# Kernel optimization log

Measured on AMD Instinct MI355X. Metric: run time of the kernel, lower is better.

## Reference

```python
import jax, jax.numpy as jnp
import numpy as np

B, T, C, H = 2, 2048, 1024, 16
HD = C // H
EPS = 1e-5


def _gelu_tanh(x):
    # 0.5*x*(1+tanh(sqrt(2/pi)*(x+0.044715*x^3)))
    c = jnp.sqrt(jnp.asarray(2.0 / np.pi, dtype=x.dtype))
    return 0.5 * x * (1.0 + jnp.tanh(c * (x + 0.044715 * x * x * x)))


def _layernorm(x, g, b):
    mu = jnp.mean(x, axis=-1, keepdims=True)
    var = jnp.mean(jnp.square(x - mu), axis=-1, keepdims=True)
    return (x - mu) * jax.lax.rsqrt(var + EPS) * g + b


def setup_inputs() -> dict:
    key = jax.random.key(0)
    ks = jax.random.split(key, 8)
    s = lambda fan_in: 1.0 / np.sqrt(fan_in)
    return {
        "x": jax.random.normal(ks[0], (B, T, C), jnp.float32),
        "ln1_g": jnp.ones((C,), jnp.float32),
        "ln1_b": jnp.zeros((C,), jnp.float32),
        "W_attn": jax.random.normal(ks[1], (C, 3 * C), jnp.float32) * s(C),
        "b_attn": jnp.zeros((3 * C,), jnp.float32),
        "W_proj": jax.random.normal(ks[2], (C, C), jnp.float32) * s(C),
        "b_proj": jnp.zeros((C,), jnp.float32),
        "ln2_g": jnp.ones((C,), jnp.float32),
        "ln2_b": jnp.zeros((C,), jnp.float32),
        "W_fc": jax.random.normal(ks[3], (C, 4 * C), jnp.float32) * s(C),
        "b_fc": jnp.zeros((4 * C,), jnp.float32),
        "W_fc2": jax.random.normal(ks[4], (4 * C, C), jnp.float32) * s(4 * C),
        "b_fc2": jnp.zeros((C,), jnp.float32),
    }


def reference(x, ln1_g, ln1_b, W_attn, b_attn, W_proj, b_proj,
              ln2_g, ln2_b, W_fc, b_fc, W_fc2, b_fc2):
    # --- attention branch (pre-LN) ---
    h = _layernorm(x, ln1_g, ln1_b)
    qkv = h @ W_attn + b_attn                      # [B,T,3C]
    q, k, v = jnp.split(qkv, 3, axis=2)
    q = q.reshape(B, T, H, HD).transpose(0, 2, 1, 3)  # [B,H,T,HD]
    k = k.reshape(B, T, H, HD).transpose(0, 2, 1, 3)
    v = v.reshape(B, T, H, HD).transpose(0, 2, 1, 3)
    att = jnp.einsum('bhqd,bhkd->bhqk', q, k) / jnp.sqrt(jnp.asarray(HD, x.dtype))
    causal = jnp.tril(jnp.ones((T, T), bool))
    att = jnp.where(causal, att, jnp.asarray(-jnp.inf, att.dtype))
    att = jax.nn.softmax(att, axis=-1)
    y = jnp.einsum('bhqk,bhkd->bhqd', att, v)      # [B,H,T,HD]
    y = y.transpose(0, 2, 1, 3).reshape(B, T, C)
    x = x + (y @ W_proj + b_proj)
    # --- MLP branch (pre-LN) ---
    h = _layernorm(x, ln2_g, ln2_b)
    h = _gelu_tanh(h @ W_fc + b_fc)
    x = x + (h @ W_fc2 + b_fc2)
    return x
```

## Files before the change

### kernel.cpp

```cpp
#include <hip/hip_runtime.h>
#include <hip/hip_bf16.h>
#include <cstdint>
#include <cstddef>

#define B_  2
#define T_  2048
#define C_  1024
#define H_  16
#define HD_ 64
#define M_TOT 4096

typedef __bf16 bf16x8 __attribute__((ext_vector_type(8)));
typedef float  f32x4  __attribute__((ext_vector_type(4)));
typedef unsigned short u16;

__device__ __forceinline__ u16 f2bf(float f) {
  __hip_bfloat16 h = __float2bfloat16(f);
  return __builtin_bit_cast(u16, h);
}

__device__ __forceinline__ void async_cp16(const u16* g, u16* l) {
  __builtin_amdgcn_global_load_lds(
      (const __attribute__((address_space(1))) void*)g,
      (__attribute__((address_space(3))) void*)l, 16, 0, 0);
}

__device__ __forceinline__ float gelu_f(float x) {
  const float z = 0.7978845608028654f * (x + 0.044715f * x * x * x);
  return x / (1.0f + __expf(-2.0f * z));
}

__device__ __forceinline__ void ln_row(
    const float* __restrict__ x, const float* __restrict__ g,
    const float* __restrict__ b, u16* __restrict__ out, int row, int tid) {
  const float4 v = reinterpret_cast<const float4*>(x)[row * 256 + tid];
  float s  = v.x + v.y + v.z + v.w;
  float sq = v.x * v.x + v.y * v.y + v.z * v.z + v.w * v.w;
#pragma unroll
  for (int off = 32; off > 0; off >>= 1) {
    s  += __shfl_xor(s, off);
    sq += __shfl_xor(sq, off);
  }
  __shared__ float red[8];
  const int wave = tid >> 6;
  if ((tid & 63) == 0) { red[wave] = s; red[4 + wave] = sq; }
  __syncthreads();
  s  = red[0] + red[1] + red[2] + red[3];
  sq = red[4] + red[5] + red[6] + red[7];
  const float mu   = s * (1.0f / 1024.0f);
  const float rstd = rsqrtf(sq * (1.0f / 1024.0f) - mu * mu + 1e-5f);
  const float4 gv = reinterpret_cast<const float4*>(g)[tid];
  const float4 bv = reinterpret_cast<const float4*>(b)[tid];
  ushort4 o;
  o.x = f2bf((v.x - mu) * rstd * gv.x + bv.x);
  o.y = f2bf((v.y - mu) * rstd * gv.y + bv.y);
  o.z = f2bf((v.z - mu) * rstd * gv.z + bv.z);
  o.w = f2bf((v.w - mu) * rstd * gv.w + bv.w);
  reinterpret_cast<ushort4*>(out)[row * 256 + tid] = o;
}

__global__ __launch_bounds__(256) void ln_bf16_kernel(
    const float* __restrict__ x, const float* __restrict__ g,
    const float* __restrict__ b, u16* __restrict__ out) {
  ln_row(x, g, b, out, blockIdx.x, threadIdx.x);
}

__global__ __launch_bounds__(256) void prep_kernel(
    const float* __restrict__ x, const float* __restrict__ ln1_g,
    const float* __restrict__ ln1_b, u16* __restrict__ h1,
    const float* __restrict__ W_attn, u16* __restrict__ wt_attn,
    const float* __restrict__ W_proj, u16* __restrict__ wt_proj,
    const float* __restrict__ W_fc,   u16* __restrict__ wt_fc,
    const float* __restrict__ W_fc2,  u16* __restrict__ wt_fc2) {
  int bid = blockIdx.x;
  if (bid < 4096) { ln_row(x, ln1_g, ln1_b, h1, bid, threadIdx.x); return; }
  bid -= 4096;
  const float* W; u16* Wt; int K, N, nx;
  if (bid < 3072)      {              W = W_attn; Wt = wt_attn; K = 1024; N = 3072; nx = 96; }
  else if (bid < 4096) { bid -= 3072; W = W_proj; Wt = wt_proj; K = 1024; N = 1024; nx = 32; }
  else if (bid < 8192) { bid -= 4096; W = W_fc;   Wt = wt_fc;   K = 1024; N = 4096; nx = 128; }
  else                 { bid -= 8192; W = W_fc2;  Wt = wt_fc2;  K = 4096; N = 1024; nx = 32; }
  const int n0 = (bid % nx) * 32, k0 = (bid / nx) * 32;
  __shared__ float tile[32][33];
  const int tx = threadIdx.x & 31;
  const int ty = threadIdx.x >> 5;
#pragma unroll
  for (int i = 0; i < 4; ++i)
    tile[ty + 8 * i][tx] = W[(k0 + ty + 8 * i) * (size_t)N + n0 + tx];
  __syncthreads();
#pragma unroll
  for (int i = 0; i < 4; ++i)
    Wt[(n0 + ty + 8 * i) * (size_t)K + k0 + tx] = f2bf(tile[tx][ty + 8 * i]);
}

template <int MODE, int BM>
__global__ __launch_bounds__(256, 2) void gemm_kernel(
    const u16* __restrict__ A, const u16* __restrict__ Bt,
    const float* __restrict__ bias, const float* __restrict__ resid,
    float* __restrict__ outf, u16* __restrict__ outb,
    u16* __restrict__ qo, u16* __restrict__ ko, u16* __restrict__ vto,
    int M, int N, int K, int logPer) {
  constexpr int MT = BM / 32;
  constexpr int AI = BM / 32;
  __shared__ __align__(16) u16 As[BM * 64];
  __shared__ __align__(16) u16 Bs[128 * 64];
  const int tid  = threadIdx.x;
  const int wave = tid >> 6, lane = tid & 63;
  const int col  = lane & 15, quad = lane >> 4;
  const int wm   = wave >> 1, wn = wave & 1;

  const int flat = blockIdx.y * gridDim.x + blockIdx.x;
  const int xcd = flat & 7, sl = flat >> 3;
  const int per = 1 << logPer;
  const int bm = (xcd << logPer) + (sl & (per - 1));
  const int bn = sl >> logPer;

  const int srow = lane >> 3, sc8 = lane & 7;
  const int kcs = (sc8 ^ srow) * 8;
  const u16* ap = A  + (size_t)(bm * BM + wave * (BM / 4) + srow) * K + kcs;
  const u16* bp = Bt + (size_t)(bn * 128 + wave * 32 + srow) * K + kcs;
  u16* as_dst = As + wave * (BM / 4) * 64;
  u16* bs_dst = Bs + wave * 2048;

  f32x4 acc[MT][4] = {};

  for (int k0 = 0; k0 < K; k0 += 64) {
    __syncthreads();
#pragma unroll
    for (int i = 0; i < AI; ++i)
      async_cp16(ap + k0 + i * 8 * (size_t)K, as_dst + i * 512);
#pragma unroll
    for (int i = 0; i < 4; ++i)
      async_cp16(bp + k0 + i * 8 * (size_t)K, bs_dst + i * 512);
    __syncthreads();
#pragma unroll
    for (int kh = 0; kh < 2; ++kh) {
      const int ks = kh * 4;
      bf16x8 af[MT], bf[4];
#pragma unroll
      for (int mt = 0; mt < MT; ++mt) {
        const int row = wm * (BM / 2) + mt * 16 + col;
        af[mt] = *reinterpret_cast<const bf16x8*>(&As[row * 64 + ((ks + quad) ^ (col & 7)) * 8]);
      }
#pragma unroll
      for (int nt = 0; nt < 4; ++nt) {
        const int row = wn * 64 + nt * 16 + col;
        bf[nt] = *reinterpret_cast<const bf16x8*>(&Bs[row * 64 + ((ks + quad) ^ (col & 7)) * 8]);
      }
#pragma unroll
      for (int mt = 0; mt < MT; ++mt)
#pragma unroll
        for (int nt = 0; nt < 4; ++nt)
          acc[mt][nt] = __builtin_amdgcn_mfma_f32_16x16x32_bf16(af[mt], bf[nt], acc[mt][nt], 0, 0, 0);
    }
  }

#pragma unroll
  for (int mt = 0; mt < MT; ++mt) {
#pragma unroll
    for (int r = 0; r < 4; ++r) {
      const int grow = bm * BM + wm * (BM / 2) + mt * 16 + quad * 4 + r;
#pragma unroll
      for (int nt = 0; nt < 4; ++nt) {
        const int gcol = bn * 128 + wn * 64 + nt * 16 + col;
        const float val = acc[mt][nt][r] + bias[gcol];
        if constexpr (MODE == 0) {
          outb[(size_t)grow * N + gcol] = f2bf(gelu_f(val));
        } else if constexpr (MODE == 1) {
          outf[(size_t)grow * N + gcol] = resid[(size_t)grow * N + gcol] + val;
        } else {
          const int which = gcol >> 10, c = gcol & 1023;
          const int hh = c >> 6, dd = c & 63;
          const int bb = grow >> 11, tt = grow & 2047;
          if (which == 0)
            qo[((bb * H_ + hh) * (size_t)T_ + tt) * HD_ + dd] = f2bf(val * 0.125f);
          else if (which == 1)
            ko[((bb * H_ + hh) * (size_t)T_ + tt) * HD_ + dd] = f2bf(val);
          else
            vto[((bb * H_ + hh) * (size_t)HD_ + dd) * T_ + tt] = f2bf(val);
        }
      }
    }
  }
}

#define PSTR 68
__global__ __launch_bounds__(256, 4) void attn_kernel(
    const u16* __restrict__ q, const u16* __restrict__ k,
    const u16* __restrict__ vt, u16* __restrict__ y) {
  const int bh  = blockIdx.x;
  const int qt  = (T_ / 64 - 1) - blockIdx.y;
  const int tid = threadIdx.x;
  const int wave = tid >> 6, lane = tid & 63;
  const int col = lane & 15, quad = lane >> 4;
  const int b = bh >> 4, h = bh & 15;
  const int r0w = qt * 64 + wave * 16;

  __shared__ __align__(16) u16 Klds[64 * PSTR];
  __shared__ __align__(16) u16 Vtlds[64 * PSTR];
  __shared__ __align__(16) u16 Plds[4 * 16 * PSTR];
  u16* pw = Plds + wave * 16 * PSTR;

  bf16x8 aq0 = *reinterpret_cast<const bf16x8*>(
      &q[((size_t)bh * T_ + r0w + col) * HD_ + quad * 8]);
  bf16x8 aq1 = *reinterpret_cast<const bf16x8*>(
      &q[((size_t)bh * T_ + r0w + col) * HD_ + 32 + quad * 8]);

  bf16x8 ones;
#pragma unroll
  for (int jj = 0; jj < 8; ++jj) ones[jj] = (__bf16)1.0f;

  f32x4 o[4] = {};
  f32x4 l_acc = {};

  const int srow = tid >> 3, spart = tid & 7;
  const u16* kbase  = k  + (size_t)bh * T_ * HD_ + (size_t)srow * HD_ + spart * 8;
  const u16* vtbase = vt + (size_t)bh * HD_ * T_ + (size_t)srow * T_ + spart * 8;

  const int kb_last = qt * 64;

  uint4 kv0 = *reinterpret_cast<const uint4*>(kbase);
  uint4 kv1 = *reinterpret_cast<const uint4*>(kbase + 32 * HD_);
  uint4 kv2 = *reinterpret_cast<const uint4*>(vtbase);
  uint4 kv3 = *reinterpret_cast<const uint4*>(vtbase + 32 * T_);

  for (int kb = 0; kb <= kb_last; kb += 64) {
    *reinterpret_cast<uint4*>(&Klds[srow * PSTR + spart * 8])         = kv0;
    *reinterpret_cast<uint4*>(&Klds[(srow + 32) * PSTR + spart * 8])  = kv1;
    *reinterpret_cast<uint4*>(&Vtlds[srow * PSTR + spart * 8])        = kv2;
    *reinterpret_cast<uint4*>(&Vtlds[(srow + 32) * PSTR + spart * 8]) = kv3;
    __syncthreads();

    if (kb < kb_last) {
      const int nk = kb + 64;
      kv0 = *reinterpret_cast<const uint4*>(kbase + (size_t)nk * HD_);
      kv1 = *reinterpret_cast<const uint4*>(kbase + (size_t)nk * HD_ + 32 * HD_);
      kv2 = *reinterpret_cast<const uint4*>(vtbase + nk);
      kv3 = *reinterpret_cast<const uint4*>(vtbase + 32 * T_ + nk);
    }

    f32x4 st[4];
#pragma unroll
    for (int n = 0; n < 4; ++n) {
      const bf16x8 ak0 = *reinterpret_cast<const bf16x8*>(&Klds[(n * 16 + col) * PSTR + quad * 8]);
      const bf16x8 ak1 = *reinterpret_cast<const bf16x8*>(&Klds[(n * 16 + col) * PSTR + 32 + quad * 8]);
      f32x4 z = {};
      z = __builtin_amdgcn_mfma_f32_16x16x32_bf16(ak0, aq0, z, 0, 0, 0);
      st[n] = __builtin_amdgcn_mfma_f32_16x16x32_bf16(ak1, aq1, z, 0, 0, 0);
    }

    const bool domask = (kb + 63 > r0w);
#pragma unroll
    for (int n = 0; n < 4; ++n) {
      ushort4 pk;
#pragma unroll
      for (int r = 0; r < 4; ++r) {
        float sv = st[n][r];
        if (domask) {
          const int key = kb + n * 16 + quad * 4 + r;
          const int row = r0w + col;
          sv = (key <= row) ? sv : -1e30f;
        }
        reinterpret_cast<u16*>(&pk)[r] = f2bf(__expf(sv));
      }
      *reinterpret_cast<ushort4*>(&pw[col * PSTR + n * 16 + quad * 4]) = pk;
    }
    __builtin_amdgcn_s_waitcnt(0xC07F);

    const bf16x8 ap0 = *reinterpret_cast<const bf16x8*>(&pw[col * PSTR + quad * 8]);
    const bf16x8 ap1 = *reinterpret_cast<const bf16x8*>(&pw[col * PSTR + 32 + quad * 8]);
    l_acc = __builtin_amdgcn_mfma_f32_16x16x32_bf16(ap0, ones, l_acc, 0, 0, 0);
    l_acc = __builtin_amdgcn_mfma_f32_16x16x32_bf16(ap1, ones, l_acc, 0, 0, 0);
#pragma unroll
    for (int n = 0; n < 4; ++n) {
      const bf16x8 bv0 = *reinterpret_cast<const bf16x8*>(&Vtlds[(n * 16 + col) * PSTR + quad * 8]);
      const bf16x8 bv1 = *reinterpret_cast<const bf16x8*>(&Vtlds[(n * 16 + col) * PSTR + 32 + quad * 8]);
      o[n] = __builtin_amdgcn_mfma_f32_16x16x32_bf16(ap0, bv0, o[n], 0, 0, 0);
      o[n] = __builtin_amdgcn_mfma_f32_16x16x32_bf16(ap1, bv1, o[n], 0, 0, 0);
    }
    __syncthreads();
  }

#pragma unroll
  for (int r = 0; r < 4; ++r) {
    const int qrow = r0w + quad * 4 + r;
    const float inv = 1.0f / l_acc[r];
#pragma unroll
    for (int n = 0; n < 4; ++n)
      y[((size_t)b * T_ + qrow) * C_ + h * HD_ + n * 16 + col] = f2bf(o[n][r] * inv);
  }
}

extern "C" void kernel_launch(void* const* d_in, const int* in_sizes, int n_in,
                              void* d_out, int out_size, void* d_ws, size_t ws_size,
                              hipStream_t stream) {
  const float* x      = (const float*)d_in[0];
  const float* ln1_g  = (const float*)d_in[1];
  const float* ln1_b  = (const float*)d_in[2];
  const float* W_attn = (const float*)d_in[3];
  const float* b_attn = (const float*)d_in[4];
  const float* W_proj = (const float*)d_in[5];
  const float* b_proj = (const float*)d_in[6];
  const float* ln2_g  = (const float*)d_in[7];
  const float* ln2_b  = (const float*)d_in[8];
  const float* W_fc   = (const float*)d_in[9];
  const float* b_fc   = (const float*)d_in[10];
  const float* W_fc2  = (const float*)d_in[11];
  const float* b_fc2  = (const float*)d_in[12];
  float* out = (float*)d_out;

  char* p = (char*)d_ws;
  auto alloc = [&](size_t bytes) {
    char* r = p;
    p += (bytes + 255) & ~(size_t)255;
    return r;
  };
  u16*   h1      = (u16*)alloc((size_t)M_TOT * C_ * 2);
  u16*   wt_attn = (u16*)alloc((size_t)3 * C_ * C_ * 2);
  u16*   wt_proj = (u16*)alloc((size_t)C_ * C_ * 2);
  u16*   wt_fc   = (u16*)alloc((size_t)4 * C_ * C_ * 2);
  u16*   wt_fc2  = (u16*)alloc((size_t)C_ * 4 * C_ * 2);
  u16*   qbuf    = (u16*)alloc((size_t)M_TOT * C_ * 2);
  u16*   kbuf    = (u16*)alloc((size_t)M_TOT * C_ * 2);
  u16*   vtbuf   = (u16*)alloc((size_t)M_TOT * C_ * 2);
  u16*   ybuf    = (u16*)alloc((size_t)M_TOT * C_ * 2);
  float* x2      = (float*)alloc((size_t)M_TOT * C_ * 4);
  u16*   h2      = (u16*)alloc((size_t)M_TOT * C_ * 2);
  u16*   act     = (u16*)alloc((size_t)M_TOT * 4 * C_ * 2);

  prep_kernel<<<16384, 256, 0, stream>>>(x, ln1_g, ln1_b, h1,
                                         W_attn, wt_attn, W_proj, wt_proj,
                                         W_fc, wt_fc, W_fc2, wt_fc2);

  gemm_kernel<3, 128><<<dim3(24, 32), 256, 0, stream>>>(h1, wt_attn, b_attn, nullptr,
                                                        nullptr, nullptr, qbuf, kbuf, vtbuf,
                                                        4096, 3072, 1024, 2);
  attn_kernel<<<dim3(32, 32), 256, 0, stream>>>(qbuf, kbuf, vtbuf, ybuf);

  gemm_kernel<1, 64><<<dim3(8, 64), 256, 0, stream>>>(ybuf, wt_proj, b_proj, x,
                                                      x2, nullptr, nullptr, nullptr, nullptr,
                                                      4096, 1024, 1024, 3);
  ln_bf16_kernel<<<M_TOT, 256, 0, stream>>>(x2, ln2_g, ln2_b, h2);

  gemm_kernel<0, 128><<<dim3(32, 32), 256, 0, stream>>>(h2, wt_fc, b_fc, nullptr,
                                                        nullptr, act, nullptr, nullptr, nullptr,
                                                        4096, 4096, 1024, 2);
  gemm_kernel<1, 64><<<dim3(8, 64), 256, 0, stream>>>(act, wt_fc2, b_fc2, x2,
                                                      out, nullptr, nullptr, nullptr, nullptr,
                                                      4096, 1024, 4096, 3);
}
```

Before: 327.2 us.

## Double-buffer GEMM LDS tiles with async prefetch of next K-step

Measured after the change: 348.1 us. 6.4% more time.

```diff
diff --git a/kernel.cpp b/kernel.cpp
--- a/kernel.cpp
+++ b/kernel.cpp
@@ -102,8 +102,11 @@
     int M, int N, int K, int logPer) {
   constexpr int MT = BM / 32;
   constexpr int AI = BM / 32;
-  __shared__ __align__(16) u16 As[BM * 64];
-  __shared__ __align__(16) u16 Bs[128 * 64];
+  constexpr int NSTG = AI + 4;
+  constexpr int WAIT_NEXT = 0xF00 | 0x70 | NSTG;
+  constexpr int WAIT_LAST = 0xF00 | 0x70;
+  __shared__ __align__(16) u16 As[2][BM * 64];
+  __shared__ __align__(16) u16 Bs[2][128 * 64];
   const int tid  = threadIdx.x;
   const int wave = tid >> 6, lane = tid & 63;
   const int col  = lane & 15, quad = lane >> 4;
@@ -119,20 +122,36 @@
   const int kcs = (sc8 ^ srow) * 8;
   const u16* ap = A  + (size_t)(bm * BM + wave * (BM / 4) + srow) * K + kcs;
   const u16* bp = Bt + (size_t)(bn * 128 + wave * 32 + srow) * K + kcs;
-  u16* as_dst = As + wave * (BM / 4) * 64;
-  u16* bs_dst = Bs + wave * 2048;
+
+  {
+    u16* ad = &As[0][wave * (BM / 4) * 64];
+    u16* bd = &Bs[0][wave * 2048];
+#pragma unroll
+    for (int i = 0; i < AI; ++i) async_cp16(ap + i * 8 * (size_t)K, ad + i * 512);
+#pragma unroll
+    for (int i = 0; i < 4; ++i)  async_cp16(bp + i * 8 * (size_t)K, bd + i * 512);
+  }
 
   f32x4 acc[MT][4] = {};
+  int cur = 0;
 
   for (int k0 = 0; k0 < K; k0 += 64) {
-    __syncthreads();
-#pragma unroll
-    for (int i = 0; i < AI; ++i)
-      async_cp16(ap + k0 + i * 8 * (size_t)K, as_dst + i * 512);
-#pragma unroll
-    for (int i = 0; i < 4; ++i)
-      async_cp16(bp + k0 + i * 8 * (size_t)K, bs_dst + i * 512);
-    __syncthreads();
+    if (k0 + 64 < K) {
+      u16* ad = &As[cur ^ 1][wave * (BM / 4) * 64];
+      u16* bd = &Bs[cur ^ 1][wave * 2048];
+#pragma unroll
+      for (int i = 0; i < AI; ++i) async_cp16(ap + (k0 + 64) + i * 8 * (size_t)K, ad + i * 512);
+#pragma unroll
+      for (int i = 0; i < 4; ++i)  async_cp16(bp + (k0 + 64) + i * 8 * (size_t)K, bd + i * 512);
+      __builtin_amdgcn_s_waitcnt(WAIT_NEXT);
+    } else {
+      __builtin_amdgcn_s_waitcnt(WAIT_LAST);
+    }
+    __builtin_amdgcn_s_barrier();
+    asm volatile("" ::: "memory");
+
+    const u16* Ac = As[cur];
+    const u16* Bc = Bs[cur];
 #pragma unroll
     for (int kh = 0; kh < 2; ++kh) {
       const int ks = kh * 4;
@@ -140,12 +159,12 @@
 #pragma unroll
       for (int mt = 0; mt < MT; ++mt) {
         const int row = wm * (BM / 2) + mt * 16 + col;
-        af[mt] = *reinterpret_cast<const bf16x8*>(&As[row * 64 + ((ks + quad) ^ (col & 7)) * 8]);
+        af[mt] = *reinterpret_cast<const bf16x8*>(&Ac[row * 64 + ((ks + quad) ^ (col & 7)) * 8]);
       }
 #pragma unroll
       for (int nt = 0; nt < 4; ++nt) {
         const int row = wn * 64 + nt * 16 + col;
-        bf[nt] = *reinterpret_cast<const bf16x8*>(&Bs[row * 64 + ((ks + quad) ^ (col & 7)) * 8]);
+        bf[nt] = *reinterpret_cast<const bf16x8*>(&Bc[row * 64 + ((ks + quad) ^ (col & 7)) * 8]);
       }
 #pragma unroll
       for (int mt = 0; mt < MT; ++mt)
@@ -153,6 +172,11 @@
         for (int nt = 0; nt < 4; ++nt)
           acc[mt][nt] = __builtin_amdgcn_mfma_f32_16x16x32_bf16(af[mt], bf[nt], acc[mt][nt], 0, 0, 0);
     }
+
+    asm volatile("" ::: "memory");
+    __builtin_amdgcn_s_waitcnt(0xC07F);
+    __builtin_amdgcn_s_barrier();
+    cur ^= 1;
   }
 
 #pragma unroll
```
